# Performance work log

Hardware: AMD Instinct MI355X
Metric: run time of the kernel (lower is better)

The kernel has to match this reference:

```python
import jax, jax.numpy as jnp
import numpy as np

B, S, D = 8, 2048, 128

def setup_inputs() -> dict:
    key = jax.random.key(0)
    kq, kk, kv, km = jax.random.split(key, 4)
    q = jax.random.normal(kq, (B, S, D), dtype=jnp.float32)
    k = jax.random.normal(kk, (B, S, D), dtype=jnp.float32)
    v = jax.random.normal(kv, (B, S, D), dtype=jnp.float32)
    mask = jax.random.randint(km, (B, S), 0, 2).astype(bool)  # True = masked out
    return {"q": q, "k": k, "v": v, "mask": mask}

def reference(q, k, v, mask):
    scaler = np.sqrt(D).astype(np.float32)
    # score[b, i, j] = <q_i, k_j> / sqrt(d_k)
    score = jnp.einsum('bik,bjk->bij', q, k) / scaler
    score = score - jnp.max(score, axis=-1, keepdims=True)
    e = jnp.exp(score)
    # mask is (B, S_kv): broadcast across query positions, zero out masked keys
    e = jnp.where(mask[:, None, :], 0.0, e)
    a = e / jnp.sum(e, axis=-1, keepdims=True)
    c = jnp.einsum('bij,bjd->bid', a, v)
    return c
```

## Files before the change

kernel.cpp:

```cpp
#include <hip/hip_runtime.h>
#include <hip/hip_fp16.h>
#include <math.h>

typedef __attribute__((ext_vector_type(8))) short short8;
typedef __attribute__((ext_vector_type(16))) float floatx16;
typedef __attribute__((ext_vector_type(2))) __bf16 bf16x2;

namespace {
constexpr int Bn = 8;
constexpr int Sn = 2048;
constexpr int Dn = 128;
constexpr int BQ = 64;
constexpr int BK = 64;
constexpr int QTILES = Sn / BQ;
constexpr int NKB = Sn / BK;
constexpr int ROWS = Bn * Sn;
constexpr int NSPLIT = 4;
constexpr float SC2 = 0.12753102063642597f;
constexpr int TILE_USH = BK * Dn;
}

#if __has_builtin(__builtin_amdgcn_exp2f)
#define EXP2(x) __builtin_amdgcn_exp2f(x)
#else
#define EXP2(x) exp2f(x)
#endif

__device__ __forceinline__ unsigned short f2bf(float x) {
  union { float f; unsigned u; } a; a.f = x;
  unsigned r = a.u + 0x7fffu + ((a.u >> 16) & 1u);
  return (unsigned short)(r >> 16);
}

__device__ __forceinline__ unsigned pack2bf(float x, float y) {
  union { bf16x2 b; unsigned u; } c;
  c.b[0] = (__bf16)x; c.b[1] = (__bf16)y;
  return c.u;
}

__device__ __forceinline__ void gl_lds16(const void* g, void* l, int lane) {
#if __has_builtin(__builtin_amdgcn_global_load_lds)
  (void)lane;
  __builtin_amdgcn_global_load_lds((const __attribute__((address_space(1))) unsigned int*)g,
                                   (__attribute__((address_space(3))) unsigned int*)l, 16, 0, 0);
#else
  *(float4*)((char*)l + lane * 16) = *(const float4*)g;
#endif
}

__global__ __launch_bounds__(256)
void prep(const float* __restrict__ kg, const float* __restrict__ vg,
          const unsigned char* __restrict__ mraw,
          unsigned short* __restrict__ Kpg, unsigned short* __restrict__ Vpg,
          float* __restrict__ mb2g) {
  __shared__ __align__(16) float Vf[16 * 136];
  const int p = blockIdx.x;
  const int b = p >> 7, q = p & 127;
  const int kb = q >> 2, k16 = q & 3;
  const int t = threadIdx.x;

  unsigned wv = ((const unsigned int*)mraw)[t];
  int any1  = __syncthreads_or((wv & 0x0000ff00u) ? 1 : 0);
  int any23 = __syncthreads_or((wv & 0xffff0000u) ? 1 : 0);
  const int mlayout = any1 ? 1 : (any23 ? 2 : 0);
  if (p < 64) {
    int idx = p * 256 + t;
    bool ms;
    if (mlayout == 1)      ms = mraw[idx] != 0;
    else if (mlayout == 2) ms = ((const float*)mraw)[idx] != 0.0f;
    else                   ms = ((const int*)mraw)[idx] != 0;
    mb2g[idx] = ms ? -1e30f : 0.0f;
  }

  const int j  = t >> 4;
  const int o8 = t & 15;
  const size_t base = ((size_t)(b * Sn + kb * 64 + k16 * 16 + j)) * 32 + o8 * 2;
  const float4* k4 = (const float4*)kg;
  const float4* v4 = (const float4*)vg;

  {
    float4 a = k4[base], bq = k4[base + 1];
    union { unsigned u[4]; short8 s8; } pk;
    pk.u[0] = pack2bf(a.x, a.y);   pk.u[1] = pack2bf(a.z, a.w);
    pk.u[2] = pack2bf(bq.x, bq.y); pk.u[3] = pack2bf(bq.z, bq.w);
    const int jl = k16 * 16 + j;
    *(short8*)(Kpg + (size_t)(b * NKB + kb) * TILE_USH + jl * 128 + ((o8 ^ (jl & 7)) * 8)) = pk.s8;
  }
  {
    float4 a = v4[base], bq = v4[base + 1];
    *(float4*)&Vf[j * 136 + o8 * 8]     = a;
    *(float4*)&Vf[j * 136 + o8 * 8 + 4] = bq;
  }
  __syncthreads();
  {
    const int d = t >> 1, h = t & 1;
    union { unsigned u[4]; short8 s8; } pv;
    #pragma unroll
    for (int i = 0; i < 4; ++i)
      pv.u[i] = pack2bf(Vf[(h * 8 + 2 * i) * 136 + d], Vf[(h * 8 + 2 * i + 1) * 136 + d]);
    const int og = k16 * 2 + h;
    *(short8*)(Vpg + (size_t)(b * NKB + kb) * TILE_USH + d * 64 + ((og ^ (d & 7)) * 8)) = pv.s8;
  }
}

template<int SPLIT, bool DIRECT>
__global__ __launch_bounds__(128, 2)
void attn_fwd(const float* __restrict__ qg,
              const unsigned short* __restrict__ Kpg,
              const unsigned short* __restrict__ Vpg,
              const float* __restrict__ mb2g,
              float* __restrict__ outg, __half* __restrict__ Op,
              float* __restrict__ Mp, float* __restrict__ Lp) {
  __shared__ __align__(16) unsigned short Khi[TILE_USH];
  __shared__ __align__(16) unsigned short Vt[TILE_USH];
  __shared__ __align__(16) unsigned short Pq[2 * 2048];

  const int tid = threadIdx.x;
  const int bid = blockIdx.x;
  const int b   = bid & 7;
  const int q0  = ((bid >> 3) & (QTILES - 1)) * BQ;
  const int s   = bid >> 8;
  const int kb0 = s * (NKB / SPLIT);
  const int kbN = kb0 + NKB / SPLIT;
  const int w   = tid >> 6;
  const int L   = tid & 63;
  const int q   = L & 31;
  const int h   = L >> 5;
  const int sw  = q & 7;

  short8 qh[8], ql[8];
  {
    const float* qrow = qg + (size_t)(b * Sn + q0 + w * 32 + q) * Dn;
    #pragma unroll
    for (int kstep = 0; kstep < 8; ++kstep) {
      float4 f0 = *(const float4*)(qrow + kstep * 16 + h * 8);
      float4 f1 = *(const float4*)(qrow + kstep * 16 + h * 8 + 4);
      float xs[8] = {f0.x, f0.y, f0.z, f0.w, f1.x, f1.y, f1.z, f1.w};
      #pragma unroll
      for (int j = 0; j < 8; ++j) {
        unsigned short hi = f2bf(xs[j]);
        union { unsigned u; float f; } hv; hv.u = ((unsigned)hi) << 16;
        qh[kstep][j] = (short)hi;
        ql[kstep][j] = (short)f2bf(xs[j] - hv.f);
      }
    }
  }

  float m_i = -INFINITY, l_i = 0.0f;
  floatx16 O32[4];
  #pragma unroll
  for (int dg = 0; dg < 4; ++dg)
    #pragma unroll
    for (int r = 0; r < 16; ++r) O32[dg][r] = 0.0f;

  unsigned short* pwave = Pq + w * 2048;
  const int stagebase = w * 8192;

  for (int kb = kb0; kb < kbN; ++kb) {
    __syncthreads();
    {
      const char* kt = (const char*)(Kpg + (size_t)(b * NKB + kb) * TILE_USH);
      const char* vt = (const char*)(Vpg + (size_t)(b * NKB + kb) * TILE_USH);
      #pragma unroll
      for (int i = 0; i < 8; ++i) {
        const int off = stagebase + i * 1024;
        gl_lds16(kt + off + L * 16, (char*)Khi + off, L);
        gl_lds16(vt + off + L * 16, (char*)Vt + off, L);
      }
    }
    __syncthreads();

    const float4* mb4 = (const float4*)(mb2g + b * Sn + kb * BK);
    float4 mbv[2][4];
    #pragma unroll
    for (int kg = 0; kg < 2; ++kg)
      #pragma unroll
      for (int ro = 0; ro < 4; ++ro) mbv[kg][ro] = mb4[kg * 8 + ro * 2 + h];

    floatx16 a32[2];
    #pragma unroll
    for (int kg = 0; kg < 2; ++kg)
      #pragma unroll
      for (int r = 0; r < 16; ++r) a32[kg][r] = 0.0f;
    #pragma unroll
    for (int kstep = 0; kstep < 8; ++kstep) {
      const int ko = ((kstep * 2 + h) ^ sw) * 8;
      #pragma unroll
      for (int kg = 0; kg < 2; ++kg) {
        short8 kf = *(const short8*)&Khi[(kg * 32 + q) * 128 + ko];
        a32[kg] = __builtin_amdgcn_mfma_f32_32x32x16_bf16(kf, qh[kstep], a32[kg], 0, 0, 0);
        a32[kg] = __builtin_amdgcn_mfma_f32_32x32x16_bf16(kf, ql[kstep], a32[kg], 0, 0, 0);
      }
    }

    #pragma unroll
    for (int kg = 0; kg < 2; ++kg)
      #pragma unroll
      for (int ro = 0; ro < 4; ++ro) {
        float4 f = mbv[kg][ro];
        a32[kg][4 * ro + 0] = fmaf(a32[kg][4 * ro + 0], SC2, f.x);
        a32[kg][4 * ro + 1] = fmaf(a32[kg][4 * ro + 1], SC2, f.y);
        a32[kg][4 * ro + 2] = fmaf(a32[kg][4 * ro + 2], SC2, f.z);
        a32[kg][4 * ro + 3] = fmaf(a32[kg][4 * ro + 3], SC2, f.w);
      }
    float mx = -INFINITY;
    #pragma unroll
    for (int kg = 0; kg < 2; ++kg)
      #pragma unroll
      for (int r = 0; r < 16; ++r) mx = fmaxf(mx, a32[kg][r]);
    mx = fmaxf(mx, __shfl_xor(mx, 32));
    const float mnew = fmaxf(m_i, mx);
    const float alpha = EXP2(m_i - mnew);
    float rs = 0.0f;
    #pragma unroll
    for (int kg = 0; kg < 2; ++kg)
      #pragma unroll
      for (int r = 0; r < 16; ++r) {
        float e = EXP2(a32[kg][r] - mnew);
        a32[kg][r] = e;
        rs += e;
      }
    rs += __shfl_xor(rs, 32);
    l_i = l_i * alpha + rs;
    m_i = mnew;

    #pragma unroll
    for (int kg = 0; kg < 2; ++kg)
      #pragma unroll
      for (int ro = 0; ro < 4; ++ro) {
        uint2 u;
        u.x = pack2bf(a32[kg][4 * ro + 0], a32[kg][4 * ro + 1]);
        u.y = pack2bf(a32[kg][4 * ro + 2], a32[kg][4 * ro + 3]);
        const int oct = kg * 4 + ro;
        *(uint2*)&pwave[q * 64 + ((oct ^ sw) * 8) + h * 4] = u;
      }

    if (!__all(alpha == 1.0f)) {
      #pragma unroll
      for (int dg = 0; dg < 4; ++dg)
        #pragma unroll
        for (int r = 0; r < 16; ++r) O32[dg][r] *= alpha;
    }

    #pragma unroll
    for (int k2 = 0; k2 < 4; ++k2) {
      const int ko = ((k2 * 2 + h) ^ sw) * 8;
      short8 pf = *(const short8*)&pwave[q * 64 + ko];
      #pragma unroll
      for (int dg = 0; dg < 4; ++dg) {
        short8 vf = *(const short8*)&Vt[(dg * 32 + q) * 64 + ko];
        O32[dg] = __builtin_amdgcn_mfma_f32_32x32x16_bf16(vf, pf, O32[dg], 0, 0, 0);
      }
    }
  }

  const int row = b * Sn + q0 + w * 32 + q;
  if constexpr (DIRECT) {
    const float inv = 1.0f / l_i;
    float* orow = outg + (size_t)row * Dn;
    #pragma unroll
    for (int dg = 0; dg < 4; ++dg)
      #pragma unroll
      for (int ro = 0; ro < 4; ++ro) {
        float4 f = make_float4(O32[dg][4 * ro] * inv,     O32[dg][4 * ro + 1] * inv,
                               O32[dg][4 * ro + 2] * inv, O32[dg][4 * ro + 3] * inv);
        *(float4*)&orow[dg * 32 + 8 * ro + 4 * h] = f;
      }
  } else {
    __half* orow = Op + ((size_t)s * ROWS + row) * Dn;
    #pragma unroll
    for (int dg = 0; dg < 4; ++dg)
      #pragma unroll
      for (int ro = 0; ro < 4; ++ro) {
        union { __half2 h2[2]; uint2 u; } pk;
        pk.h2[0] = __floats2half2_rn(O32[dg][4 * ro],     O32[dg][4 * ro + 1]);
        pk.h2[1] = __floats2half2_rn(O32[dg][4 * ro + 2], O32[dg][4 * ro + 3]);
        *(uint2*)&orow[dg * 32 + 8 * ro + 4 * h] = pk.u;
      }
    if (h == 0) {
      Mp[s * ROWS + row] = m_i;
      Lp[s * ROWS + row] = l_i;
    }
  }
}

__global__ __launch_bounds__(256)
void attn_combine(const __half* __restrict__ Op, const float* __restrict__ Mp,
                  const float* __restrict__ Lp, float4* __restrict__ out4) {
  const int gid = blockIdx.x * 256 + threadIdx.x;
  const int row = gid >> 5;
  const int c4  = gid & 31;
  float ms[NSPLIT];
  float m = -INFINITY;
  #pragma unroll
  for (int s = 0; s < NSPLIT; ++s) { ms[s] = Mp[s * ROWS + row]; m = fmaxf(m, ms[s]); }
  float l = 0.0f;
  float4 acc = make_float4(0.f, 0.f, 0.f, 0.f);
  #pragma unroll
  for (int s = 0; s < NSPLIT; ++s) {
    float wgt = EXP2(ms[s] - m);
    l = fmaf(Lp[s * ROWS + row], wgt, l);
    union { uint2 u; __half2 h2[2]; } pk;
    pk.u = ((const uint2*)Op)[(size_t)(s * ROWS + row) * 32 + c4];
    float2 f0 = __half22float2(pk.h2[0]);
    float2 f1 = __half22float2(pk.h2[1]);
    acc.x = fmaf(f0.x, wgt, acc.x);
    acc.y = fmaf(f0.y, wgt, acc.y);
    acc.z = fmaf(f1.x, wgt, acc.z);
    acc.w = fmaf(f1.y, wgt, acc.w);
  }
  float inv = 1.0f / l;
  out4[(size_t)row * 32 + c4] = make_float4(acc.x * inv, acc.y * inv, acc.z * inv, acc.w * inv);
}

extern "C" void kernel_launch(void* const* d_in, const int* in_sizes, int n_in,
                              void* d_out, int out_size, void* d_ws, size_t ws_size,
                              hipStream_t stream) {
  const float* q = (const float*)d_in[0];
  const float* k = (const float*)d_in[1];
  const float* v = (const float*)d_in[2];
  const unsigned char* m = (const unsigned char*)d_in[3];
  float* out = (float*)d_out;
  (void)in_sizes; (void)n_in; (void)out_size;

  constexpr size_t OPB = (size_t)NSPLIT * ROWS * Dn * sizeof(__half);
  constexpr size_t MLB = (size_t)NSPLIT * ROWS * sizeof(float);
  constexpr size_t KPB = (size_t)Bn * NKB * TILE_USH * 2;
  constexpr size_t MBB = (size_t)ROWS * sizeof(float);

  char* ws = (char*)d_ws;
  if (ws_size >= OPB + 2 * MLB + 2 * KPB + MBB) {
    __half* Op = (__half*)ws;
    float* Mp = (float*)(ws + OPB);
    float* Lp = (float*)(ws + OPB + MLB);
    unsigned short* Kp = (unsigned short*)(ws + OPB + 2 * MLB);
    unsigned short* Vp = (unsigned short*)(ws + OPB + 2 * MLB + KPB);
    float* mb2 = (float*)(ws + OPB + 2 * MLB + 2 * KPB);
    prep<<<dim3(Bn * NKB * 4), dim3(256), 0, stream>>>(k, v, m, Kp, Vp, mb2);
    attn_fwd<NSPLIT, false><<<dim3(Bn * QTILES * NSPLIT), dim3(128), 0, stream>>>(
        q, Kp, Vp, mb2, out, Op, Mp, Lp);
    attn_combine<<<dim3(ROWS * 32 / 256), dim3(256), 0, stream>>>(
        Op, Mp, Lp, (float4*)out);
  } else if (ws_size >= 2 * KPB + MBB) {
    unsigned short* Kp = (unsigned short*)ws;
    unsigned short* Vp = (unsigned short*)(ws + KPB);
    float* mb2 = (float*)(ws + 2 * KPB);
    prep<<<dim3(Bn * NKB * 4), dim3(256), 0, stream>>>(k, v, m, Kp, Vp, mb2);
    attn_fwd<1, true><<<dim3(Bn * QTILES), dim3(128), 0, stream>>>(
        q, Kp, Vp, mb2, out, nullptr, nullptr, nullptr);
  }
}
```

Before: 118.3 us.

## Double-buffer K/V tiles in LDS and double the query tile per block

```diff
diff --git a/kernel.cpp b/kernel.cpp
--- a/kernel.cpp
+++ b/kernel.cpp
@@ -10,7 +10,7 @@
 constexpr int Bn = 8;
 constexpr int Sn = 2048;
 constexpr int Dn = 128;
-constexpr int BQ = 64;
+constexpr int BQ = 128;
 constexpr int BK = 64;
 constexpr int QTILES = Sn / BQ;
 constexpr int NKB = Sn / BK;
@@ -104,22 +104,22 @@
 }
 
 template<int SPLIT, bool DIRECT>
-__global__ __launch_bounds__(128, 2)
+__global__ __launch_bounds__(256, 2)
 void attn_fwd(const float* __restrict__ qg,
               const unsigned short* __restrict__ Kpg,
               const unsigned short* __restrict__ Vpg,
               const float* __restrict__ mb2g,
               float* __restrict__ outg, __half* __restrict__ Op,
               float* __restrict__ Mp, float* __restrict__ Lp) {
-  __shared__ __align__(16) unsigned short Khi[TILE_USH];
-  __shared__ __align__(16) unsigned short Vt[TILE_USH];
-  __shared__ __align__(16) unsigned short Pq[2 * 2048];
+  __shared__ __align__(16) unsigned short Khi[2][TILE_USH];
+  __shared__ __align__(16) unsigned short Vt[2][TILE_USH];
+  __shared__ __align__(16) unsigned short Pq[4 * 2048];
 
   const int tid = threadIdx.x;
   const int bid = blockIdx.x;
   const int b   = bid & 7;
   const int q0  = ((bid >> 3) & (QTILES - 1)) * BQ;
-  const int s   = bid >> 8;
+  const int s   = bid >> 7;
   const int kb0 = s * (NKB / SPLIT);
   const int kbN = kb0 + NKB / SPLIT;
   const int w   = tid >> 6;
@@ -128,6 +128,10 @@
   const int h   = L >> 5;
   const int sw  = q & 7;
 
+  const char* ktile = (const char*)(Kpg + (size_t)b * NKB * TILE_USH);
+  const char* vtile = (const char*)(Vpg + (size_t)b * NKB * TILE_USH);
+  const int stagebase = w * 4096;
+
   short8 qh[8], ql[8];
   {
     const float* qrow = qg + (size_t)(b * Sn + q0 + w * 32 + q) * Dn;
@@ -154,21 +158,35 @@
     for (int r = 0; r < 16; ++r) O32[dg][r] = 0.0f;
 
   unsigned short* pwave = Pq + w * 2048;
-  const int stagebase = w * 8192;
+
+  {
+    const char* kt = ktile + (size_t)kb0 * (TILE_USH * 2);
+    const char* vt = vtile + (size_t)kb0 * (TILE_USH * 2);
+    #pragma unroll
+    for (int i = 0; i < 4; ++i) {
+      const int off = stagebase + i * 1024;
+      gl_lds16(kt + off + L * 16, (char*)Khi[0] + off, L);
+      gl_lds16(vt + off + L * 16, (char*)Vt[0] + off, L);
+    }
+  }
 
   for (int kb = kb0; kb < kbN; ++kb) {
+    const int cur = (kb - kb0) & 1;
     __syncthreads();
-    {
-      const char* kt = (const char*)(Kpg + (size_t)(b * NKB + kb) * TILE_USH);
-      const char* vt = (const char*)(Vpg + (size_t)(b * NKB + kb) * TILE_USH);
-      #pragma unroll
-      for (int i = 0; i < 8; ++i) {
+
+    if (kb + 1 < kbN) {
+      const char* kt = ktile + (size_t)(kb + 1) * (TILE_USH * 2);
+      const char* vt = vtile + (size_t)(kb + 1) * (TILE_USH * 2);
+      #pragma unroll
+      for (int i = 0; i < 4; ++i) {
         const int off = stagebase + i * 1024;
-        gl_lds16(kt + off + L * 16, (char*)Khi + off, L);
-        gl_lds16(vt + off + L * 16, (char*)Vt + off, L);
-      }
-    }
-    __syncthreads();
+        gl_lds16(kt + off + L * 16, (char*)Khi[cur ^ 1] + off, L);
+        gl_lds16(vt + off + L * 16, (char*)Vt[cur ^ 1] + off, L);
+      }
+    }
+
+    const unsigned short* Kc = Khi[cur];
+    const unsigned short* Vc = Vt[cur];
 
     const float4* mb4 = (const float4*)(mb2g + b * Sn + kb * BK);
     float4 mbv[2][4];
@@ -187,7 +205,7 @@
       const int ko = ((kstep * 2 + h) ^ sw) * 8;
       #pragma unroll
       for (int kg = 0; kg < 2; ++kg) {
-        short8 kf = *(const short8*)&Khi[(kg * 32 + q) * 128 + ko];
+        short8 kf = *(const short8*)&Kc[(kg * 32 + q) * 128 + ko];
         a32[kg] = __builtin_amdgcn_mfma_f32_32x32x16_bf16(kf, qh[kstep], a32[kg], 0, 0, 0);
         a32[kg] = __builtin_amdgcn_mfma_f32_32x32x16_bf16(kf, ql[kstep], a32[kg], 0, 0, 0);
       }
@@ -248,7 +266,7 @@
       short8 pf = *(const short8*)&pwave[q * 64 + ko];
       #pragma unroll
       for (int dg = 0; dg < 4; ++dg) {
-        short8 vf = *(const short8*)&Vt[(dg * 32 + q) * 64 + ko];
+        short8 vf = *(const short8*)&Vc[(dg * 32 + q) * 64 + ko];
         O32[dg] = __builtin_amdgcn_mfma_f32_32x32x16_bf16(vf, pf, O32[dg], 0, 0, 0);
       }
     }
@@ -337,7 +355,7 @@
     unsigned short* Vp = (unsigned short*)(ws + OPB + 2 * MLB + KPB);
     float* mb2 = (float*)(ws + OPB + 2 * MLB + 2 * KPB);
     prep<<<dim3(Bn * NKB * 4), dim3(256), 0, stream>>>(k, v, m, Kp, Vp, mb2);
-    attn_fwd<NSPLIT, false><<<dim3(Bn * QTILES * NSPLIT), dim3(128), 0, stream>>>(
+    attn_fwd<NSPLIT, false><<<dim3(Bn * QTILES * NSPLIT), dim3(256), 0, stream>>>(
         q, Kp, Vp, mb2, out, Op, Mp, Lp);
     attn_combine<<<dim3(ROWS * 32 / 256), dim3(256), 0, stream>>>(
         Op, Mp, Lp, (float4*)out);
@@ -346,7 +364,7 @@
     unsigned short* Vp = (unsigned short*)(ws + KPB);
     float* mb2 = (float*)(ws + 2 * KPB);
     prep<<<dim3(Bn * NKB * 4), dim3(256), 0, stream>>>(k, v, m, Kp, Vp, mb2);
-    attn_fwd<1, true><<<dim3(Bn * QTILES), dim3(128), 0, stream>>>(
+    attn_fwd<1, true><<<dim3(Bn * QTILES), dim3(256), 0, stream>>>(
         q, Kp, Vp, mb2, out, nullptr, nullptr, nullptr);
   }
 }
```

Result: faster. 114.4 us (-3.3%).
